# Kernel tuning notes

Hardware: AMD Instinct MI355X
Metric: run time of the kernel (lower is better)

## Reference

```python
import jax, jax.numpy as jnp
import numpy as np

N_HEAD = 16
D_MODEL = 2048
ROPE_BASE = 10000.0


def setup_inputs() -> dict:
    key = jax.random.key(0)
    k1, k2, k3 = jax.random.split(key, 3)
    b, s, d = 2, 2048, D_MODEL
    x = jax.random.normal(k1, (b, s, d), dtype=jnp.float32)
    # torch nn.Linear init scale ~ 1/sqrt(fan_in); keep activations sane
    W_qkv = jax.random.normal(k2, (3 * d, d), dtype=jnp.float32) * (d ** -0.5)
    W_o = jax.random.normal(k3, (d, d), dtype=jnp.float32) * (d ** -0.5)
    return {"x": x, "W_qkv": W_qkv, "W_o": W_o}


def _rotate_half(x):
    x1, x2 = jnp.split(x, 2, axis=-1)
    return jnp.concatenate((-x2, x1), axis=-1)


def _rope_cos_sin(seq_len, d_head, dtype):
    inv_freq = 1.0 / (ROPE_BASE ** (jnp.arange(0, d_head, 2, dtype=jnp.float32) / d_head))
    t = jnp.arange(seq_len, dtype=jnp.float32)
    freqs = jnp.einsum("i,j->ij", t, inv_freq)          # [s, d_head/2]
    emb = jnp.concatenate((freqs, freqs), axis=-1)       # [s, d_head]
    return jnp.cos(emb).astype(dtype)[None, None], jnp.sin(emb).astype(dtype)[None, None]


def reference(x, W_qkv, W_o):
    b, s, d = x.shape
    h = N_HEAD
    dh = d // h
    qkv = x @ W_qkv.T                                    # [b, s, 3d]
    qkv = qkv.reshape(b, s, 3, h, dh)
    q, k, v = (jnp.transpose(qkv[:, :, i], (0, 2, 1, 3)) for i in range(3))  # [b, h, s, dh]
    cos, sin = _rope_cos_sin(s, dh, x.dtype)
    q = q * cos + _rotate_half(q) * sin
    k = k * cos + _rotate_half(k) * sin
    scale = dh ** -0.5
    scores = jnp.einsum("bhqd,bhkd->bhqk", q, k) * scale  # [b, h, s, s]
    causal = jnp.tril(jnp.ones((s, s), dtype=bool))
    scores = jnp.where(causal[None, None], scores, jnp.finfo(scores.dtype).min)
    attn = jax.nn.softmax(scores, axis=-1)
    z = jnp.einsum("bhqk,bhkd->bhqd", attn, v)            # [b, h, s, dh]
    z = jnp.transpose(z, (0, 2, 1, 3)).reshape(b, s, d)
    return z @ W_o.T
```

## Files before the change

kernel.cpp:

```cpp
#include <hip/hip_runtime.h>
#include <stdint.h>
#include <stddef.h>

typedef __attribute__((ext_vector_type(8))) short bf16x8;
typedef __attribute__((ext_vector_type(4))) float f32x4;
typedef __attribute__((ext_vector_type(16))) float f32x16;
typedef __attribute__((ext_vector_type(4))) unsigned int u32x4;

#define AS1 __attribute__((address_space(1)))
#define AS3 __attribute__((address_space(3)))

__device__ __forceinline__ void gll16(const void* g, void* l) {
  __builtin_amdgcn_global_load_lds((const AS1 unsigned int*)g, (AS3 unsigned int*)l, 16, 0, 0);
}

__device__ __forceinline__ uint16_t f2bf(float f) {
  uint32_t u = __builtin_bit_cast(uint32_t, f);
  u += 0x7fffu + ((u >> 16) & 1u);
  return (uint16_t)(u >> 16);
}
__device__ __forceinline__ float bf2f(uint16_t h) {
  uint32_t u = ((uint32_t)h) << 16;
  return __builtin_bit_cast(float, u);
}
__device__ __forceinline__ uint32_t cvtpk(float lo, float hi) {
  uint32_t r;
  asm("v_cvt_pk_bf16_f32 %0, %1, %2" : "=v"(r) : "v"(lo), "v"(hi));
  return r;
}

#define BARRIER() do { asm volatile("" ::: "memory"); __builtin_amdgcn_s_barrier(); asm volatile("" ::: "memory"); } while (0)

__global__ void cvt_all(const float* __restrict__ x, const float* __restrict__ wqkv,
                        const float* __restrict__ wo,
                        uint16_t* __restrict__ xb, uint16_t* __restrict__ wqkvb,
                        uint16_t* __restrict__ wob) {
  int i = blockIdx.x * blockDim.x + threadIdx.x;
  const float* in; uint16_t* out; int off;
  if (i < 1048576)      { in = x;    out = xb;    off = i; }
  else if (i < 2621440) { in = wqkv; out = wqkvb; off = i - 1048576; }
  else                  { in = wo;   out = wob;   off = i - 2621440; }
  float4 a = reinterpret_cast<const float4*>(in)[2 * off];
  float4 b = reinterpret_cast<const float4*>(in)[2 * off + 1];
  union { uint16_t h[8]; u32x4 v; } u;
  u.h[0] = f2bf(a.x); u.h[1] = f2bf(a.y); u.h[2] = f2bf(a.z); u.h[3] = f2bf(a.w);
  u.h[4] = f2bf(b.x); u.h[5] = f2bf(b.y); u.h[6] = f2bf(b.z); u.h[7] = f2bf(b.w);
  reinterpret_cast<u32x4*>(out)[off] = u.v;
}

__global__ void rope_table(float* __restrict__ cosT, float* __restrict__ sinT) {
  int idx = blockIdx.x * blockDim.x + threadIdx.x;
  int s = idx >> 6, i = idx & 63;
  float invf = expf(-(float)i * (9.2103403719761836f / 64.0f));
  float f = (float)s * invf;
  cosT[idx] = cosf(f);
  sinT[idx] = sinf(f);
}

__global__ void rope_apply2(uint16_t* __restrict__ Qb, uint16_t* __restrict__ Kb,
                            const float* __restrict__ cosT, const float* __restrict__ sinT) {
  int idx = blockIdx.x * blockDim.x + threadIdx.x;
  uint16_t* buf = (idx < 4194304) ? Qb : Kb;
  int id = idx & 4194303;
  int i = id & 63;
  int s = (id >> 6) & 2047;
  int bh = id >> 17;
  size_t base = ((size_t)bh * 2048 + s) * 128;
  float x0 = bf2f(buf[base + i]);
  float x1 = bf2f(buf[base + i + 64]);
  float c = cosT[(s << 6) + i], sn = sinT[(s << 6) + i];
  buf[base + i]      = f2bf(x0 * c - x1 * sn);
  buf[base + i + 64] = f2bf(x1 * c + x0 * sn);
}

__global__ __launch_bounds__(512, 2) void gemm_qkv(
    const uint16_t* __restrict__ A,
    const uint16_t* __restrict__ B,
    uint16_t* __restrict__ Qb, uint16_t* __restrict__ Kb, uint16_t* __restrict__ Vt) {
  extern __shared__ uint16_t L[];
  const int t = threadIdx.x, lane = t & 63, w = t >> 6;
  const int fr = lane & 15, fg = lane >> 4;
  const int wm = w >> 2, wn = w & 3;
  const int flat = blockIdx.y * 16 + blockIdx.x;
  const int swz = (flat & 7) * 64 + (flat >> 3);
  const int m0 = (swz & 15) * 256, n0 = (swz >> 4) * 192;

  f32x4 acc[8][3];
#pragma unroll
  for (int i = 0; i < 8; i++)
#pragma unroll
    for (int j = 0; j < 3; j++) acc[i][j] = (f32x4)(0.0f);

#define STA(kt, half)                                                             \
  do {                                                                            \
    if ((kt) < 32) {                                                              \
      int g0_ = m0 + (half) * 128;                                                \
      uint16_t* dst_ = &L[((kt) & 1) * 28672 + (half) * 8192];                    \
      _Pragma("unroll")                                                           \
      for (int j_ = 0; j_ < 2; ++j_) {                                            \
        int c_ = t + j_ * 512;                                                    \
        int row_ = c_ >> 3, cc_ = c_ & 7, scc_ = cc_ ^ (row_ & 7);                \
        gll16(&A[(size_t)(g0_ + row_) * 2048 + (kt) * 64 + scc_ * 8],             \
              &dst_[(c_ & ~63) * 8]);                                             \
      }                                                                           \
    }                                                                             \
  } while (0)

#define STB(kt)                                                                   \
  do {                                                                            \
    if ((kt) < 32) {                                                              \
      uint16_t* dst_ = &L[((kt) & 1) * 28672 + 16384];                            \
      _Pragma("unroll")                                                           \
      for (int j_ = 0; j_ < 3; ++j_) {                                            \
        int c_ = t + j_ * 512;                                                    \
        int row_ = c_ >> 3, cc_ = c_ & 7, scc_ = cc_ ^ (row_ & 7);                \
        gll16(&B[(size_t)(n0 + row_) * 2048 + (kt) * 64 + scc_ * 8],              \
              &dst_[(c_ & ~63) * 8]);                                             \
      }                                                                           \
    }                                                                             \
  } while (0)

  auto LDA4 = [&](bf16x8 (&af)[8], int buf, int mh) {
#pragma unroll
    for (int mi = 0; mi < 4; ++mi)
#pragma unroll
      for (int ks = 0; ks < 2; ++ks) {
        int lr = (mh * 4 + mi) * 16 + fr;
        int ck = (ks * 4 + fg) ^ (lr & 7);
        af[mi * 2 + ks] = *(const bf16x8*)&L[buf * 28672 + wm * 8192 + lr * 64 + ck * 8];
      }
  };
  auto LDB = [&](bf16x8* bfr, int buf, int ni0, int nn) {
#pragma unroll
    for (int ni = 0; ni < 2; ++ni) {
      if (ni >= nn) break;
#pragma unroll
      for (int ks = 0; ks < 2; ++ks) {
        int rn = wn * 48 + (ni0 + ni) * 16 + fr;
        int ck = (ks * 4 + fg) ^ (rn & 7);
        bfr[ni * 2 + ks] = *(const bf16x8*)&L[buf * 28672 + 16384 + rn * 64 + ck * 8];
      }
    }
  };
  auto MF = [&](bf16x8 (&af)[8], bf16x8* bfr, int mh, int ni0, int nn) {
    __builtin_amdgcn_s_setprio(1);
#pragma unroll
    for (int mi = 0; mi < 4; ++mi)
#pragma unroll
      for (int ni = 0; ni < 2; ++ni) {
        if (ni >= nn) break;
#pragma unroll
        for (int ks = 0; ks < 2; ++ks)
          acc[mh * 4 + mi][ni0 + ni] = __builtin_amdgcn_mfma_f32_16x16x32_bf16(
              af[mi * 2 + ks], bfr[ni * 2 + ks], acc[mh * 4 + mi][ni0 + ni], 0, 0, 0);
      }
    __builtin_amdgcn_s_setprio(0);
  };

  STA(0, 0); STA(0, 1); STB(0); STA(1, 0);
  asm volatile("s_waitcnt vmcnt(2)" ::: "memory");
  BARRIER();

  for (int tl = 0; tl < 32; ++tl) {
    const int buf = tl & 1;
    bf16x8 af[8], bA[4], bB[4];
    LDA4(af, buf, 0); LDB(bA, buf, 0, 2); STA(tl + 1, 1);
    BARRIER(); MF(af, bA, 0, 0, 2); BARRIER();
    LDB(bB, buf, 2, 1); STB(tl + 1);
    BARRIER(); MF(af, bB, 0, 2, 1); BARRIER();
    LDA4(af, buf, 1);
    BARRIER(); MF(af, bA, 1, 0, 2); BARRIER();
    STA(tl + 2, 0);
    BARRIER(); MF(af, bB, 1, 2, 1);
    if (tl < 30) asm volatile("s_waitcnt vmcnt(2)" ::: "memory");
    else         asm volatile("s_waitcnt vmcnt(0)" ::: "memory");
    BARRIER();
  }
#undef STA
#undef STB

#pragma unroll
  for (int mi = 0; mi < 8; ++mi) {
#pragma unroll
    for (int ni = 0; ni < 3; ++ni) {
      int ng = n0 + wn * 48 + ni * 16 + fr;
      int head = (ng >> 7) & 15, dd = ng & 127;
      if (ng < 4096) {
        uint16_t* dst = (ng < 2048) ? Qb : Kb;
#pragma unroll
        for (int r = 0; r < 4; r++) {
          int mg = m0 + wm * 128 + mi * 16 + fg * 4 + r;
          int b = mg >> 11, si = mg & 2047;
          dst[((size_t)(b * 16 + head) * 2048 + si) * 128 + dd] = f2bf(acc[mi][ni][r]);
        }
      } else {
        uint2 pv = make_uint2(cvtpk(acc[mi][ni][0], acc[mi][ni][1]),
                              cvtpk(acc[mi][ni][2], acc[mi][ni][3]));
        int mg = m0 + wm * 128 + mi * 16 + fg * 4;
        int b = mg >> 11, si = mg & 2047;
        *(uint2*)&Vt[((size_t)(b * 16 + head) * 128 + dd) * 2048 + si] = pv;
      }
    }
  }
}

__global__ __launch_bounds__(512, 2) void gemm_out_k(
    const uint16_t* __restrict__ A,
    const uint16_t* __restrict__ B,
    float* __restrict__ C) {
  extern __shared__ uint16_t L[];
  const int t = threadIdx.x, lane = t & 63, w = t >> 6;
  const int fr = lane & 15, fg = lane >> 4;
  const int wm = w >> 2, wn = w & 3;
  const int flat = blockIdx.y * 16 + blockIdx.x;
  const int swz = (flat & 7) * 32 + (flat >> 3);
  const int m0 = (swz & 15) * 256, n0 = (swz >> 4) * 128;

  f32x4 acc[8][2];
#pragma unroll
  for (int i = 0; i < 8; i++)
#pragma unroll
    for (int j = 0; j < 2; j++) acc[i][j] = (f32x4)(0.0f);

#define STA(kt, half)                                                             \
  do {                                                                            \
    if ((kt) < 32) {                                                              \
      int g0_ = m0 + (half) * 128;                                                \
      uint16_t* dst_ = &L[((kt) & 1) * 24576 + (half) * 8192];                    \
      _Pragma("unroll")                                                           \
      for (int j_ = 0; j_ < 2; ++j_) {                                            \
        int c_ = t + j_ * 512;                                                    \
        int row_ = c_ >> 3, cc_ = c_ & 7, scc_ = cc_ ^ (row_ & 7);                \
        gll16(&A[(size_t)(g0_ + row_) * 2048 + (kt) * 64 + scc_ * 8],             \
              &dst_[(c_ & ~63) * 8]);                                             \
      }                                                                           \
    }                                                                             \
  } while (0)

#define STB(kt)                                                                   \
  do {                                                                            \
    if ((kt) < 32) {                                                              \
      uint16_t* dst_ = &L[((kt) & 1) * 24576 + 16384];                            \
      _Pragma("unroll")                                                           \
      for (int j_ = 0; j_ < 2; ++j_) {                                            \
        int c_ = t + j_ * 512;                                                    \
        int row_ = c_ >> 3, cc_ = c_ & 7, scc_ = cc_ ^ (row_ & 7);                \
        gll16(&B[(size_t)(n0 + row_) * 2048 + (kt) * 64 + scc_ * 8],              \
              &dst_[(c_ & ~63) * 8]);                                             \
      }                                                                           \
    }                                                                             \
  } while (0)

  auto LDA4 = [&](bf16x8 (&af)[8], int buf, int mh) {
#pragma unroll
    for (int mi = 0; mi < 4; ++mi)
#pragma unroll
      for (int ks = 0; ks < 2; ++ks) {
        int lr = (mh * 4 + mi) * 16 + fr;
        int ck = (ks * 4 + fg) ^ (lr & 7);
        af[mi * 2 + ks] = *(const bf16x8*)&L[buf * 24576 + wm * 8192 + lr * 64 + ck * 8];
      }
  };
  auto LDB1 = [&](bf16x8 (&bfr)[2], int buf, int ni) {
#pragma unroll
    for (int ks = 0; ks < 2; ++ks) {
      int rn = wn * 32 + ni * 16 + fr;
      int ck = (ks * 4 + fg) ^ (rn & 7);
      bfr[ks] = *(const bf16x8*)&L[buf * 24576 + 16384 + rn * 64 + ck * 8];
    }
  };
  auto MF1 = [&](bf16x8 (&af)[8], bf16x8 (&bfr)[2], int mh, int ni) {
    __builtin_amdgcn_s_setprio(1);
#pragma unroll
    for (int mi = 0; mi < 4; ++mi)
#pragma unroll
      for (int ks = 0; ks < 2; ++ks)
        acc[mh * 4 + mi][ni] = __builtin_amdgcn_mfma_f32_16x16x32_bf16(
            af[mi * 2 + ks], bfr[ks], acc[mh * 4 + mi][ni], 0, 0, 0);
    __builtin_amdgcn_s_setprio(0);
  };

  STA(0, 0); STA(0, 1); STB(0); STA(1, 0);
  asm volatile("s_waitcnt vmcnt(2)" ::: "memory");
  BARRIER();

  for (int tl = 0; tl < 32; ++tl) {
    const int buf = tl & 1;
    bf16x8 af[8], bA[2], bB[2];
    LDA4(af, buf, 0); LDB1(bA, buf, 0); STA(tl + 1, 1);
    BARRIER(); MF1(af, bA, 0, 0); BARRIER();
    LDB1(bB, buf, 1); STB(tl + 1);
    BARRIER(); MF1(af, bB, 0, 1); BARRIER();
    LDA4(af, buf, 1);
    BARRIER(); MF1(af, bA, 1, 0); BARRIER();
    STA(tl + 2, 0);
    BARRIER(); MF1(af, bB, 1, 1);
    if (tl < 30) asm volatile("s_waitcnt vmcnt(2)" ::: "memory");
    else         asm volatile("s_waitcnt vmcnt(0)" ::: "memory");
    BARRIER();
  }
#undef STA
#undef STB

#pragma unroll
  for (int mi = 0; mi < 8; ++mi) {
#pragma unroll
    for (int ni = 0; ni < 2; ++ni) {
      int ng = n0 + wn * 32 + ni * 16 + fr;
#pragma unroll
      for (int r = 0; r < 4; r++) {
        int mg = m0 + wm * 128 + mi * 16 + fg * 4 + r;
        C[(size_t)mg * 2048 + ng] = acc[mi][ni][r];
      }
    }
  }
}

__device__ __forceinline__ bf16x8 mk_pa(uint32_t p0, uint32_t p1, uint32_t p2, uint32_t p3, int hi) {
  uint32_t x0 = (uint32_t)__shfl_xor((int)p0, 32, 64);
  uint32_t x1 = (uint32_t)__shfl_xor((int)p1, 32, 64);
  uint32_t x2 = (uint32_t)__shfl_xor((int)p2, 32, 64);
  uint32_t x3 = (uint32_t)__shfl_xor((int)p3, 32, 64);
  u32x4 v;
  v[0] = hi ? x2 : p0;
  v[1] = hi ? x3 : p1;
  v[2] = hi ? p2 : x0;
  v[3] = hi ? p3 : x1;
  return __builtin_bit_cast(bf16x8, v);
}

__global__ __launch_bounds__(256, 2) void attn_kernel(
    const uint16_t* __restrict__ Qb, const uint16_t* __restrict__ Kb,
    const uint16_t* __restrict__ Vt, uint16_t* __restrict__ zb) {
  __shared__ uint16_t Ksh[2][64 * 128];
  __shared__ uint16_t Vsh[2][128 * 64];

  const int t = threadIdx.x, lane = t & 63, w = t >> 6;
  const int l31 = lane & 31, hi = lane >> 5;
  const int bx = blockIdx.x, bh = blockIdx.y;
  const int qt = (bh & 16) ? (15 - bx) : bx;
  const int q0 = qt * 128;
  const int qg = q0 + w * 32 + l31;
  const size_t hbase = (size_t)bh * 2048 * 128;
  const float scale2 = 0.08838834764831845f * 1.4426950408889634f;

#define ATT_STAGE(kt, buf)                                                        \
  do {                                                                            \
    const uint16_t* Kg_ = Kb + hbase + (size_t)(kt) * 64 * 128;                   \
    const uint16_t* Vg_ = Vt + hbase + (size_t)(kt) * 64;                         \
    _Pragma("unroll")                                                             \
    for (int i_ = 0; i_ < 4; i_++) {                                              \
      int c_ = t + i_ * 256;                                                      \
      { int row_ = c_ >> 4, cc_ = c_ & 15, scc_ = cc_ ^ (row_ & 7);               \
        gll16(&Kg_[row_ * 128 + scc_ * 8], &Ksh[buf][(c_ & ~63) * 8]); }          \
      { int r_ = c_ >> 3, cc_ = c_ & 7, scc_ = cc_ ^ (r_ & 7);                    \
        gll16(&Vg_[(size_t)r_ * 2048 + scc_ * 8], &Vsh[buf][(c_ & ~63) * 8]); }   \
    }                                                                             \
  } while (0)

  bf16x8 qf[8];
#pragma unroll
  for (int dc = 0; dc < 8; ++dc)
    qf[dc] = *(const bf16x8*)&Qb[hbase + (size_t)qg * 128 + dc * 16 + hi * 8];

  f32x16 oacc[4];
#pragma unroll
  for (int i = 0; i < 4; i++) oacc[i] = (f32x16)(0.0f);
  float mrow = -1e30f, lrow = 0.0f;

  const int ktiles = 2 * qt + 2;
  ATT_STAGE(0, 0);
  asm volatile("s_waitcnt vmcnt(0)" ::: "memory");
  BARRIER();

  for (int kt = 0; kt < ktiles; ++kt) {
    const int cur = kt & 1;
    if (kt + 1 < ktiles) ATT_STAGE(kt + 1, cur ^ 1);

    const int kv_base = kt * 64;
    if (kv_base <= q0 + w * 32 + 31) {
      f32x16 s0 = (f32x16)(0.0f), s1 = (f32x16)(0.0f);
      __builtin_amdgcn_s_setprio(1);
#pragma unroll
      for (int dc = 0; dc < 8; ++dc) {
        int ch = dc * 2 + hi;
        bf16x8 k0 = *(const bf16x8*)&Ksh[cur][l31 * 128 + ((ch ^ (l31 & 7)) * 8)];
        bf16x8 k1 = *(const bf16x8*)&Ksh[cur][(32 + l31) * 128 + ((ch ^ (l31 & 7)) * 8)];
        s0 = __builtin_amdgcn_mfma_f32_32x32x16_bf16(k0, qf[dc], s0, 0, 0, 0);
        s1 = __builtin_amdgcn_mfma_f32_32x32x16_bf16(k1, qf[dc], s1, 0, 0, 0);
      }
      __builtin_amdgcn_s_setprio(0);

      const bool need_mask = (kv_base + 63 > q0 + w * 32);
#pragma unroll
      for (int reg = 0; reg < 16; ++reg) {
        int koff = (reg & 3) + 8 * (reg >> 2) + 4 * hi;
        float a0 = s0[reg] * scale2, a1 = s1[reg] * scale2;
        if (need_mask) {
          if (kv_base + koff > qg) a0 = -1e30f;
          if (kv_base + 32 + koff > qg) a1 = -1e30f;
        }
        s0[reg] = a0; s1[reg] = a1;
      }

      float m8[8];
#pragma unroll
      for (int i = 0; i < 8; ++i)
        m8[i] = fmaxf(fmaxf(s0[i], s0[i + 8]), fmaxf(s1[i], s1[i + 8]));
      float pmax = fmaxf(fmaxf(fmaxf(m8[0], m8[4]), fmaxf(m8[1], m8[5])),
                         fmaxf(fmaxf(m8[2], m8[6]), fmaxf(m8[3], m8[7])));
      pmax = fmaxf(pmax, __shfl_xor(pmax, 32, 64));

      bool defer = __all(pmax <= mrow + 8.0f);
      if (!defer) {
        float mnew = fmaxf(mrow, pmax);
        float al = exp2f(mrow - mnew);
        lrow *= al;
#pragma unroll
        for (int reg = 0; reg < 16; ++reg) {
          int src = (reg & 3) + 8 * (reg >> 2) + 4 * hi;
          float ar = __shfl(al, src, 64);
#pragma unroll
          for (int n = 0; n < 4; ++n) oacc[n][reg] *= ar;
        }
        mrow = mnew;
      }

      float ps0 = 0.0f, ps1 = 0.0f, ps2 = 0.0f, ps3 = 0.0f;
      uint32_t pk0[8], pk1[8];
#pragma unroll
      for (int i = 0; i < 8; ++i) {
        float a = exp2f(s0[2 * i] - mrow), b = exp2f(s0[2 * i + 1] - mrow);
        ps0 += a; ps1 += b;
        pk0[i] = cvtpk(a, b);
        float c = exp2f(s1[2 * i] - mrow), d = exp2f(s1[2 * i + 1] - mrow);
        ps2 += c; ps3 += d;
        pk1[i] = cvtpk(c, d);
      }
      float ps = (ps0 + ps1) + (ps2 + ps3);
      ps += __shfl_xor(ps, 32, 64);
      lrow += ps;

      bf16x8 pa[4];
      pa[0] = mk_pa(pk0[0], pk0[1], pk0[2], pk0[3], hi);
      pa[1] = mk_pa(pk0[4], pk0[5], pk0[6], pk0[7], hi);
      pa[2] = mk_pa(pk1[0], pk1[1], pk1[2], pk1[3], hi);
      pa[3] = mk_pa(pk1[4], pk1[5], pk1[6], pk1[7], hi);

      __builtin_amdgcn_s_setprio(1);
#pragma unroll
      for (int ksl = 0; ksl < 4; ++ksl) {
        int ch = ksl * 2 + hi;
#pragma unroll
        for (int n = 0; n < 4; ++n) {
          int d = n * 32 + l31;
          bf16x8 vf = *(const bf16x8*)&Vsh[cur][d * 64 + ((ch ^ (d & 7)) * 8)];
          oacc[n] = __builtin_amdgcn_mfma_f32_32x32x16_bf16(pa[ksl], vf, oacc[n], 0, 0, 0);
        }
      }
      __builtin_amdgcn_s_setprio(0);
    }

    asm volatile("s_waitcnt vmcnt(0)" ::: "memory");
    BARRIER();
  }
#undef ATT_STAGE

  const int b = bh >> 4, h = bh & 15;
#pragma unroll
  for (int reg = 0; reg < 16; ++reg) {
    int rloc = (reg & 3) + 8 * (reg >> 2) + 4 * hi;
    float linv = 1.0f / __shfl(lrow, rloc, 64);
    int rowg = q0 + w * 32 + rloc;
    size_t base = ((size_t)b * 2048 + rowg) * 2048 + h * 128 + l31;
#pragma unroll
    for (int n = 0; n < 4; ++n)
      zb[base + n * 32] = f2bf(oacc[n][reg] * linv);
  }
}

extern "C" void kernel_launch(void* const* d_in, const int* in_sizes, int n_in,
                              void* d_out, int out_size, void* d_ws, size_t ws_size,
                              hipStream_t stream) {
  const float* x    = (const float*)d_in[0];
  const float* Wqkv = (const float*)d_in[1];
  const float* Wo   = (const float*)d_in[2];
  float* out = (float*)d_out;
  char* ws = (char*)d_ws;

  uint16_t* Qb    = (uint16_t*)(ws + 0);
  uint16_t* Kb    = (uint16_t*)(ws + 16777216);
  uint16_t* Vt    = (uint16_t*)(ws + 33554432);
  uint16_t* xb    = (uint16_t*)(ws + 50331648);
  uint16_t* zb    = (uint16_t*)(ws + 50331648);
  uint16_t* wqkvb = (uint16_t*)(ws + 67108864);
  uint16_t* wob   = (uint16_t*)(ws + 92274688);
  float*    cosT  = (float*)   (ws + 100663296);
  float*    sinT  = (float*)   (ws + 101187584);

  cvt_all<<<12288, 256, 0, stream>>>(x, Wqkv, Wo, xb, wqkvb, wob);
  rope_table<<<512, 256, 0, stream>>>(cosT, sinT);

  gemm_qkv<<<dim3(16, 32), 512, 114688, stream>>>(xb, wqkvb, Qb, Kb, Vt);

  rope_apply2<<<32768, 256, 0, stream>>>(Qb, Kb, cosT, sinT);

  attn_kernel<<<dim3(16, 32), 256, 0, stream>>>(Qb, Kb, Vt, zb);

  gemm_out_k<<<dim3(16, 16), 512, 98304, stream>>>(zb, wob, out);
}
```

Baseline: 277.4 us.

## Fuse rope table into convert kernel, vectorize rope apply, fold Q scale into GEMM

The rope cos/sin table build moves into the conversion kernel as extra blocks, which removes one launch. rope_apply2 now handles four elements per thread with vector loads and packed bf16 conversion, cutting its thread count by four. The softmax scale is folded into Q at the QKV GEMM epilogue, so the attention loop no longer multiplies every score. The trailing wait and barrier after the final KV tile are skipped. Scaling Q before bf16 rounding slightly changes numerics, and because RoPE is linear the pre-scaled Q still gives the correct result.

Result: faster. 261.5 us (-5.7%).

```diff
diff --git a/kernel.cpp b/kernel.cpp
--- a/kernel.cpp
+++ b/kernel.cpp
@@ -31,46 +31,59 @@
 
 #define BARRIER() do { asm volatile("" ::: "memory"); __builtin_amdgcn_s_barrier(); asm volatile("" ::: "memory"); } while (0)
 
+#define QSCALE (0.08838834764831845f * 1.4426950408889634f)
+
 __global__ void cvt_all(const float* __restrict__ x, const float* __restrict__ wqkv,
                         const float* __restrict__ wo,
                         uint16_t* __restrict__ xb, uint16_t* __restrict__ wqkvb,
-                        uint16_t* __restrict__ wob) {
-  int i = blockIdx.x * blockDim.x + threadIdx.x;
+                        uint16_t* __restrict__ wob,
+                        float* __restrict__ cosT, float* __restrict__ sinT) {
+  int b = blockIdx.x;
+  if (b >= 12288) {
+    int idx = (b - 12288) * 256 + threadIdx.x;
+    int s = idx >> 6, i = idx & 63;
+    float invf = expf(-(float)i * (9.2103403719761836f / 64.0f));
+    float f = (float)s * invf;
+    cosT[idx] = cosf(f);
+    sinT[idx] = sinf(f);
+    return;
+  }
+  int i = b * 256 + threadIdx.x;
   const float* in; uint16_t* out; int off;
   if (i < 1048576)      { in = x;    out = xb;    off = i; }
   else if (i < 2621440) { in = wqkv; out = wqkvb; off = i - 1048576; }
   else                  { in = wo;   out = wob;   off = i - 2621440; }
   float4 a = reinterpret_cast<const float4*>(in)[2 * off];
-  float4 b = reinterpret_cast<const float4*>(in)[2 * off + 1];
+  float4 c = reinterpret_cast<const float4*>(in)[2 * off + 1];
   union { uint16_t h[8]; u32x4 v; } u;
   u.h[0] = f2bf(a.x); u.h[1] = f2bf(a.y); u.h[2] = f2bf(a.z); u.h[3] = f2bf(a.w);
-  u.h[4] = f2bf(b.x); u.h[5] = f2bf(b.y); u.h[6] = f2bf(b.z); u.h[7] = f2bf(b.w);
+  u.h[4] = f2bf(c.x); u.h[5] = f2bf(c.y); u.h[6] = f2bf(c.z); u.h[7] = f2bf(c.w);
   reinterpret_cast<u32x4*>(out)[off] = u.v;
-}
-
-__global__ void rope_table(float* __restrict__ cosT, float* __restrict__ sinT) {
-  int idx = blockIdx.x * blockDim.x + threadIdx.x;
-  int s = idx >> 6, i = idx & 63;
-  float invf = expf(-(float)i * (9.2103403719761836f / 64.0f));
-  float f = (float)s * invf;
-  cosT[idx] = cosf(f);
-  sinT[idx] = sinf(f);
 }
 
 __global__ void rope_apply2(uint16_t* __restrict__ Qb, uint16_t* __restrict__ Kb,
                             const float* __restrict__ cosT, const float* __restrict__ sinT) {
   int idx = blockIdx.x * blockDim.x + threadIdx.x;
-  uint16_t* buf = (idx < 4194304) ? Qb : Kb;
-  int id = idx & 4194303;
-  int i = id & 63;
-  int s = (id >> 6) & 2047;
-  int bh = id >> 17;
+  uint16_t* buf = (idx < 1048576) ? Qb : Kb;
+  int id = idx & 1048575;
+  int i = (id & 15) * 4;
+  int s = (id >> 4) & 2047;
+  int bh = id >> 15;
   size_t base = ((size_t)bh * 2048 + s) * 128;
-  float x0 = bf2f(buf[base + i]);
-  float x1 = bf2f(buf[base + i + 64]);
-  float c = cosT[(s << 6) + i], sn = sinT[(s << 6) + i];
-  buf[base + i]      = f2bf(x0 * c - x1 * sn);
-  buf[base + i + 64] = f2bf(x1 * c + x0 * sn);
+  uint2 lo = *(const uint2*)&buf[base + i];
+  uint2 hi = *(const uint2*)&buf[base + i + 64];
+  float4 c  = *(const float4*)&cosT[(s << 6) + i];
+  float4 sn = *(const float4*)&sinT[(s << 6) + i];
+  float x00 = bf2f((uint16_t)(lo.x & 0xffff)), x01 = bf2f((uint16_t)(lo.x >> 16));
+  float x02 = bf2f((uint16_t)(lo.y & 0xffff)), x03 = bf2f((uint16_t)(lo.y >> 16));
+  float x10 = bf2f((uint16_t)(hi.x & 0xffff)), x11 = bf2f((uint16_t)(hi.x >> 16));
+  float x12 = bf2f((uint16_t)(hi.y & 0xffff)), x13 = bf2f((uint16_t)(hi.y >> 16));
+  uint2 olo = make_uint2(cvtpk(x00 * c.x - x10 * sn.x, x01 * c.y - x11 * sn.y),
+                         cvtpk(x02 * c.z - x12 * sn.z, x03 * c.w - x13 * sn.w));
+  uint2 ohi = make_uint2(cvtpk(x10 * c.x + x00 * sn.x, x11 * c.y + x01 * sn.y),
+                         cvtpk(x12 * c.z + x02 * sn.z, x13 * c.w + x03 * sn.w));
+  *(uint2*)&buf[base + i]      = olo;
+  *(uint2*)&buf[base + i + 64] = ohi;
 }
 
 __global__ __launch_bounds__(512, 2) void gemm_qkv(
@@ -187,11 +200,12 @@
       int head = (ng >> 7) & 15, dd = ng & 127;
       if (ng < 4096) {
         uint16_t* dst = (ng < 2048) ? Qb : Kb;
+        float sc = (ng < 2048) ? QSCALE : 1.0f;
 #pragma unroll
         for (int r = 0; r < 4; r++) {
           int mg = m0 + wm * 128 + mi * 16 + fg * 4 + r;
           int b = mg >> 11, si = mg & 2047;
-          dst[((size_t)(b * 16 + head) * 2048 + si) * 128 + dd] = f2bf(acc[mi][ni][r]);
+          dst[((size_t)(b * 16 + head) * 2048 + si) * 128 + dd] = f2bf(acc[mi][ni][r] * sc);
         }
       } else {
         uint2 pv = make_uint2(cvtpk(acc[mi][ni][0], acc[mi][ni][1]),
@@ -342,7 +356,6 @@
   const int q0 = qt * 128;
   const int qg = q0 + w * 32 + l31;
   const size_t hbase = (size_t)bh * 2048 * 128;
-  const float scale2 = 0.08838834764831845f * 1.4426950408889634f;
 
 #define ATT_STAGE(kt, buf)                                                        \
   do {                                                                            \
@@ -391,16 +404,13 @@
       }
       __builtin_amdgcn_s_setprio(0);
 
-      const bool need_mask = (kv_base + 63 > q0 + w * 32);
-#pragma unroll
-      for (int reg = 0; reg < 16; ++reg) {
-        int koff = (reg & 3) + 8 * (reg >> 2) + 4 * hi;
-        float a0 = s0[reg] * scale2, a1 = s1[reg] * scale2;
-        if (need_mask) {
-          if (kv_base + koff > qg) a0 = -1e30f;
-          if (kv_base + 32 + koff > qg) a1 = -1e30f;
+      if (kv_base + 63 > q0 + w * 32) {
+#pragma unroll
+        for (int reg = 0; reg < 16; ++reg) {
+          int koff = (reg & 3) + 8 * (reg >> 2) + 4 * hi;
+          if (kv_base + koff > qg) s0[reg] = -1e30f;
+          if (kv_base + 32 + koff > qg) s1[reg] = -1e30f;
         }
-        s0[reg] = a0; s1[reg] = a1;
       }
 
       float m8[8];
@@ -461,8 +471,10 @@
       __builtin_amdgcn_s_setprio(0);
     }
 
-    asm volatile("s_waitcnt vmcnt(0)" ::: "memory");
-    BARRIER();
+    if (kt + 1 < ktiles) {
+      asm volatile("s_waitcnt vmcnt(0)" ::: "memory");
+      BARRIER();
+    }
   }
 #undef ATT_STAGE
 
@@ -498,12 +510,11 @@
   float*    cosT  = (float*)   (ws + 100663296);
   float*    sinT  = (float*)   (ws + 101187584);
 
-  cvt_all<<<12288, 256, 0, stream>>>(x, Wqkv, Wo, xb, wqkvb, wob);
-  rope_table<<<512, 256, 0, stream>>>(cosT, sinT);
+  cvt_all<<<12800, 256, 0, stream>>>(x, Wqkv, Wo, xb, wqkvb, wob, cosT, sinT);
 
   gemm_qkv<<<dim3(16, 32), 512, 114688, stream>>>(xb, wqkvb, Qb, Kb, Vt);
 
-  rope_apply2<<<32768, 256, 0, stream>>>(Qb, Kb, cosT, sinT);
+  rope_apply2<<<8192, 256, 0, stream>>>(Qb, Kb, cosT, sinT);
 
   attn_kernel<<<dim3(16, 32), 256, 0, stream>>>(Qb, Kb, Vt, zb);
 
```
